# Kernel optimization log

Hardware: AMD Instinct MI355X
Metric: run time of the kernel (lower is better)

The kernel has to match this reference:

```python
import jax, jax.numpy as jnp
import numpy as np

N_NODES = 100000
N_EDGES = 3200000
F_IN = 128
F_OUT = 16


def setup_inputs() -> dict:
    key = jax.random.key(0)
    k1, k2, k3, k4, k5 = jax.random.split(key, 5)
    x = jax.random.normal(k1, (N_NODES, F_IN), dtype=jnp.float32)
    edge_index = jax.random.randint(k2, (2, N_EDGES), 0, N_NODES, dtype=jnp.int64)
    edge_weights = jax.random.uniform(k3, (N_EDGES,), dtype=jnp.float32)
    W = jax.random.normal(k4, (F_IN, F_OUT), dtype=jnp.float32) / np.sqrt(F_IN)
    b = jax.random.normal(k5, (F_OUT,), dtype=jnp.float32)
    return {"x": x, "edge_index": edge_index, "edge_weights": edge_weights, "W": W, "b": b}


def reference(x, edge_index, edge_weights, W, b):
    # GCNConv: out = D^{-1/2} (A + I) D^{-1/2} X W + b  (weighted edges, self-loops)
    n = x.shape[0]
    row = edge_index[0]  # source nodes
    col = edge_index[1]  # target nodes (aggregation destination)
    # add self-loops with weight 1.0 (GCNConv default)
    loop = jnp.arange(n, dtype=row.dtype)
    row_f = jnp.concatenate([row, loop])
    col_f = jnp.concatenate([col, loop])
    ew = jnp.concatenate([edge_weights, jnp.ones((n,), dtype=edge_weights.dtype)])
    # symmetric normalization: deg over destination, norm = d^{-1/2}[row] * w * d^{-1/2}[col]
    deg = jax.ops.segment_sum(ew, col_f, num_segments=n)
    dinv = jnp.where(deg > 0, jax.lax.rsqrt(deg), 0.0)
    norm = dinv[row_f] * ew * dinv[col_f]  # [E+N]
    h = x @ W  # [N, F_OUT] dense projection before propagation
    msgs = h[row_f] * norm[:, None]  # gather + scale, [E+N, F_OUT]
    out = jax.ops.segment_sum(msgs, col_f, num_segments=n)  # scatter-add
    return out + b
```

## Files before the change

### kernel.cpp

```cpp
#include <hip/hip_runtime.h>

#define N_NODES 100000
#define N_EDGES 3200000
#define F_IN 128
#define F_OUT 16

#define NSEG 512
#define EPS (N_EDGES / NSEG)
#define EPT 13
#define NBUCK 512
#define NPB 196
#define CAPR 7424
#define RPT 29
#define GEMM32 ((N_NODES + 31) / 32)
#define PULL_BLOCKS 2048

#define OFF_CUR   0x000000u
#define OFF_NPTR  0x010000u
#define OFF_NCNT  0x080000u
#define OFF_DINV  0x0F0000u
#define OFF_HH    0x160000u
#define OFF_GG    0x780000u
#define OFF_CSR   0xB00000u
#define WS_NEEDED ((size_t)0x1000000 + (size_t)N_EDGES * 8)

__device__ __forceinline__ unsigned short f2bf(float f) {
    unsigned u = __float_as_uint(f);
    unsigned r = (u + 0x7FFFu + ((u >> 16) & 1u)) >> 16;
    return (unsigned short)r;
}
__device__ __forceinline__ float bf2f(unsigned short v) {
    return __uint_as_float((unsigned)v << 16);
}


__global__ void __launch_bounds__(512) k_binA(const int* __restrict__ row,
                                              const int* __restrict__ col,
                                              const float* __restrict__ ew,
                                              int* __restrict__ cursor,
                                              int2* __restrict__ csr,
                                              const float* __restrict__ x,
                                              const float* __restrict__ W,
                                              float* __restrict__ h) {
    __shared__ int smem[2048];
    int tid = threadIdx.x;
    if (blockIdx.x < NSEG) {
        int* lcnt = smem;
        int* gofs = smem + 512;
        int e0 = blockIdx.x * EPS;
        lcnt[tid] = 0;
        __syncthreads();

        int2 rec[EPT];
        int meta[EPT];
#pragma unroll
        for (int k = 0; k < EPT; ++k) {
            int i = k * 512 + tid;
            if (k < EPT - 1 || i < EPS) {
                int e = e0 + i;
                int r = row[e];
                int c = col[e];
                float w = ew[e];
                int bk = c / NPB;
                int pos = atomicAdd(&lcnt[bk], 1);
                rec[k] = make_int2((r << 8) | (c - bk * NPB), __float_as_int(w));
                meta[k] = (bk << 16) | pos;
            }
        }
        __syncthreads();

        int v = lcnt[tid];
        gofs[tid] = tid * CAPR + atomicAdd(&cursor[tid], v);
        __syncthreads();

#pragma unroll
        for (int k = 0; k < EPT; ++k) {
            int i = k * 512 + tid;
            if (k < EPT - 1 || i < EPS) {
                int m = meta[k];
                csr[gofs[m >> 16] + (m & 0xFFFF)] = rec[k];
            }
        }
    } else {
        float* Ws = (float*)smem;
        for (int i = tid; i < F_IN * F_OUT; i += 512) Ws[i] = W[i];
        __syncthreads();
        int n = (blockIdx.x - NSEG) * 32 + (tid >> 4);
        int j = tid & 15;
        if (n >= N_NODES) return;
        const float4* xr = (const float4*)(x + (size_t)n * F_IN);
        float acc = 0.0f;
#pragma unroll
        for (int k4 = 0; k4 < F_IN / 4; ++k4) {
            float4 xv = xr[k4];
            int k = k4 * 4;
            acc += xv.x * Ws[(k + 0) * F_OUT + j];
            acc += xv.y * Ws[(k + 1) * F_OUT + j];
            acc += xv.z * Ws[(k + 2) * F_OUT + j];
            acc += xv.w * Ws[(k + 3) * F_OUT + j];
        }
        h[(size_t)n * F_OUT + j] = acc;
    }
}

__global__ void __launch_bounds__(256) k_sortB(const int* __restrict__ cursor,
                                               int2* __restrict__ csr,
                                               const float* __restrict__ h,
                                               float* __restrict__ dinv,
                                               unsigned short* __restrict__ gb,
                                               int* __restrict__ nodeptr,
                                               int* __restrict__ ncnt) {
    __shared__ int cnt[256];
    __shared__ int basel[256];
    __shared__ int wtot[4];
    __shared__ float dl[256];
    int tid = threadIdx.x;
    int b = blockIdx.x;
    int c0 = b * NPB;
    int rb = b * CAPR;
    int total = cursor[b];
    if (total > CAPR) total = CAPR;

    cnt[tid] = 0;
    __syncthreads();

    int2 rec[RPT];
    int pos[RPT];
#pragma unroll
    for (int k = 0; k < RPT; ++k) {
        int i = k * 256 + tid;
        if (i < total) {
            rec[k] = csr[rb + i];
            pos[k] = atomicAdd(&cnt[rec[k].x & 255], 1);
        }
    }
    __syncthreads();

    int v = cnt[tid];
    int inc = v;
#pragma unroll
    for (int off = 1; off < 64; off <<= 1) {
        int t = __shfl_up(inc, off);
        if ((tid & 63) >= off) inc += t;
    }
    if ((tid & 63) == 63) wtot[tid >> 6] = inc;
    __syncthreads();
    int woff = 0;
#pragma unroll
    for (int k = 0; k < 4; ++k)
        if (k < (tid >> 6)) woff += wtot[k];
    int excl = woff + inc - v;
    int n = c0 + tid;
    if (tid < NPB && n < N_NODES) {
        nodeptr[n] = rb + excl;
        ncnt[n] = v;
    }
    basel[tid] = excl;
    __syncthreads();

#pragma unroll
    for (int k = 0; k < RPT; ++k) {
        int i = k * 256 + tid;
        if (i < total) {
            int cl = rec[k].x & 255;
            csr[rb + basel[cl] + pos[k]] = make_int2(rec[k].x >> 8, rec[k].y);
        }
    }
    __syncthreads();

    float d = 0.0f;
    if (tid < NPB && n < N_NODES) {
        float s0 = 1.0f, s1 = 0.0f, s2 = 0.0f, s3 = 0.0f;
        const int2* run = csr + rb + excl;
        int k = 0;
        for (; k + 4 <= v; k += 4) {
            s0 += __int_as_float(run[k + 0].y);
            s1 += __int_as_float(run[k + 1].y);
            s2 += __int_as_float(run[k + 2].y);
            s3 += __int_as_float(run[k + 3].y);
        }
        for (; k < v; ++k) s0 += __int_as_float(run[k].y);
        float s = (s0 + s1) + (s2 + s3);
        d = rsqrtf(s);
        dinv[n] = d;
    }
    dl[tid] = d;
    __syncthreads();
    for (int i = tid; i < NPB * F_OUT; i += 256) {
        int idx = c0 * F_OUT + i;
        if (idx < N_NODES * F_OUT) gb[idx] = f2bf(dl[i >> 4] * h[idx]);
    }
}

__global__ void __launch_bounds__(256) k_pull5(const int* __restrict__ nodeptr,
                                               const int* __restrict__ ncnt,
                                               const int2* __restrict__ csr,
                                               const unsigned short* __restrict__ gb,
                                               const float* __restrict__ dinv,
                                               const float* __restrict__ bias,
                                               float* __restrict__ out) {
    int wid = threadIdx.x >> 6;
    int lane = threadIdx.x & 63;
    int half = lane >> 5;
    int l32 = lane & 31;
    int l4 = lane & 15;
    int fr = ((l4 & 1) << 3) | ((l4 & 2) << 1) | ((l4 & 4) >> 1) | ((l4 & 8) >> 3);
    float bj = bias[fr];
    const int NPAIR = (N_NODES + 1) / 2;
    for (int q = blockIdx.x * 4 + wid; q < NPAIR; q += PULL_BLOCKS * 4) {
        int n = q * 2 + half;
        bool valid = (n < N_NODES);
        int p0 = valid ? nodeptr[n] : 0;
        int c = valid ? ncnt[n] : 0;
        float acc[16];
#pragma unroll
        for (int k = 0; k < 16; ++k) acc[k] = 0.0f;
        int2 rec = (l32 < c) ? csr[p0 + l32] : make_int2(0, 0);
        for (int base = 0; base < c; base += 32) {
            int2 cur = rec;
            int ni = base + 32 + l32;
            rec = (ni < c) ? csr[p0 + ni] : make_int2(0, 0);
            float w = __int_as_float(cur.y);
            const uint4* gr = (const uint4*)(gb + ((size_t)cur.x << 4));
            uint4 qa = gr[0];
            uint4 qb = gr[1];
            acc[0]  += w * __uint_as_float(qa.x << 16);
            acc[1]  += w * __uint_as_float(qa.x & 0xFFFF0000u);
            acc[2]  += w * __uint_as_float(qa.y << 16);
            acc[3]  += w * __uint_as_float(qa.y & 0xFFFF0000u);
            acc[4]  += w * __uint_as_float(qa.z << 16);
            acc[5]  += w * __uint_as_float(qa.z & 0xFFFF0000u);
            acc[6]  += w * __uint_as_float(qa.w << 16);
            acc[7]  += w * __uint_as_float(qa.w & 0xFFFF0000u);
            acc[8]  += w * __uint_as_float(qb.x << 16);
            acc[9]  += w * __uint_as_float(qb.x & 0xFFFF0000u);
            acc[10] += w * __uint_as_float(qb.y << 16);
            acc[11] += w * __uint_as_float(qb.y & 0xFFFF0000u);
            acc[12] += w * __uint_as_float(qb.z << 16);
            acc[13] += w * __uint_as_float(qb.z & 0xFFFF0000u);
            acc[14] += w * __uint_as_float(qb.w << 16);
            acc[15] += w * __uint_as_float(qb.w & 0xFFFF0000u);
        }
        bool b1 = (lane & 1) != 0;
#pragma unroll
        for (int k = 0; k < 8; ++k) {
            float keep = b1 ? acc[k + 8] : acc[k];
            float send = b1 ? acc[k] : acc[k + 8];
            acc[k] = keep + __shfl_xor(send, 1);
        }
        bool b2 = (lane & 2) != 0;
#pragma unroll
        for (int k = 0; k < 4; ++k) {
            float keep = b2 ? acc[k + 4] : acc[k];
            float send = b2 ? acc[k] : acc[k + 4];
            acc[k] = keep + __shfl_xor(send, 2);
        }
        bool b4 = (lane & 4) != 0;
#pragma unroll
        for (int k = 0; k < 2; ++k) {
            float keep = b4 ? acc[k + 2] : acc[k];
            float send = b4 ? acc[k] : acc[k + 2];
            acc[k] = keep + __shfl_xor(send, 4);
        }
        bool b8 = (lane & 8) != 0;
        {
            float keep = b8 ? acc[1] : acc[0];
            float send = b8 ? acc[0] : acc[1];
            acc[0] = keep + __shfl_xor(send, 8);
        }
        acc[0] += __shfl_xor(acc[0], 16);
        if (l32 < 16 && valid) {
            float d = dinv[n];
            float gs = bf2f(gb[(size_t)n * F_OUT + fr]);
            out[(size_t)n * F_OUT + fr] = bj + d * (gs + acc[0]);
        }
    }
}


#define EDGE_BLOCKS_FB ((N_EDGES + 255) / 256)
#define GEMM_BLOCKS_FB ((N_NODES + 15) / 16)
__global__ void k_init_fb(float* __restrict__ deg) {
    int i = blockIdx.x * blockDim.x + threadIdx.x;
    if (i < N_NODES) deg[i] = 1.0f;
}
__global__ void k_fused_fb(const int* __restrict__ col, const float* __restrict__ ew,
                           float* __restrict__ deg, const float* __restrict__ x,
                           const float* __restrict__ W, float* __restrict__ h) {
    int b3 = blockIdx.x / 3;
    int r3 = blockIdx.x % 3;
    if (r3 < 2) {
        int e = (b3 * 2 + r3) * 256 + threadIdx.x;
        if (e < N_EDGES) atomicAdd(&deg[col[e]], ew[e]);
    } else {
        __shared__ float Ws[F_IN * F_OUT];
        int tid = threadIdx.x;
        for (int i = tid; i < F_IN * F_OUT; i += 256) Ws[i] = W[i];
        __syncthreads();
        int n = b3 * 16 + (tid >> 4);
        int j = tid & 15;
        if (n >= N_NODES) return;
        const float4* xr = (const float4*)(x + (size_t)n * F_IN);
        float acc = 0.0f;
#pragma unroll
        for (int k4 = 0; k4 < F_IN / 4; ++k4) {
            float4 xv = xr[k4];
            int k = k4 * 4;
            acc += xv.x * Ws[(k + 0) * F_OUT + j];
            acc += xv.y * Ws[(k + 1) * F_OUT + j];
            acc += xv.z * Ws[(k + 2) * F_OUT + j];
            acc += xv.w * Ws[(k + 3) * F_OUT + j];
        }
        h[(size_t)n * F_OUT + j] = acc;
    }
}
__global__ void k_final_fb(float* __restrict__ deg, const float* __restrict__ h,
                           const float* __restrict__ b, float* __restrict__ g,
                           float* __restrict__ out) {
    int i = blockIdx.x * blockDim.x + threadIdx.x;
    int n = i >> 4;
    int j = i & 15;
    if (n >= N_NODES) return;
    float d = rsqrtf(deg[n]);
    if (j == 0) deg[n] = d;
    float gg = d * h[i];
    g[i] = gg;
    out[i] = b[j] + d * gg;
}
__global__ void k_scatter_fb(const int* __restrict__ row, const int* __restrict__ col,
                             const float* __restrict__ ew, const float* __restrict__ dinv,
                             const float* __restrict__ g, float* __restrict__ out) {
    long long tid = (long long)blockIdx.x * blockDim.x + threadIdx.x;
    int e = (int)(tid >> 4);
    int j = (int)(tid & 15);
    if (e >= N_EDGES) return;
    int c = col[e];
    float norm = ew[e] * dinv[c];
    atomicAdd(&out[(size_t)c * F_OUT + j], g[(size_t)row[e] * F_OUT + j] * norm);
}

extern "C" void kernel_launch(void* const* d_in, const int* in_sizes, int n_in,
                              void* d_out, int out_size, void* d_ws, size_t ws_size,
                              hipStream_t stream) {
    const float* x  = (const float*)d_in[0];
    const int*   ei = (const int*)d_in[1];
    const float* ew = (const float*)d_in[2];
    const float* W  = (const float*)d_in[3];
    const float* b  = (const float*)d_in[4];
    float* out = (float*)d_out;

    const int* row = ei;
    const int* col = ei + N_EDGES;

    char* ws = (char*)d_ws;
    dim3 blk(256);

    if (ws_size >= WS_NEEDED) {
        int*   cur  = (int*)(ws + OFF_CUR);
        int*   nptr = (int*)(ws + OFF_NPTR);
        int*   ncnt = (int*)(ws + OFF_NCNT);
        float* dinv = (float*)(ws + OFF_DINV);
        float* h    = (float*)(ws + OFF_HH);
        unsigned short* gb = (unsigned short*)(ws + OFF_GG);
        int2*  csr  = (int2*)(ws + OFF_CSR);

        hipMemsetAsync(cur, 0, NBUCK * sizeof(int), stream);
        k_binA<<<NSEG + GEMM32, 512, 0, stream>>>(row, col, ew, cur, csr, x, W, h);
        k_sortB<<<NBUCK, blk, 0, stream>>>(cur, csr, h, dinv, gb, nptr, ncnt);
        k_pull5<<<PULL_BLOCKS, blk, 0, stream>>>(nptr, ncnt, csr, gb, dinv, b, out);
    } else {
        float* deg = (float*)ws;
        float* h   = (float*)(ws + (1u << 20));
        float* g   = (float*)(ws + (8u << 20));
        k_init_fb<<<(N_NODES + 255) / 256, blk, 0, stream>>>(deg);
        k_fused_fb<<<EDGE_BLOCKS_FB + GEMM_BLOCKS_FB, blk, 0, stream>>>(col, ew, deg, x, W, h);
        k_final_fb<<<(N_NODES * F_OUT + 255) / 256, blk, 0, stream>>>(deg, h, b, g, out);
        long long total = (long long)N_EDGES * F_OUT;
        k_scatter_fb<<<(unsigned)((total + 255) / 256), blk, 0, stream>>>(row, col, ew, deg, g, out);
    }
}
```

Baseline: 224.4 us.

## Fuse bin, sort, and pull stages into one cooperative kernel with grid syncs

Replaces the memset plus three kernel launches with a single cooperative kernel of 512 blocks of 512 threads. It zeroes the cursors, bins edges, computes the projection, sorts each bucket and builds the degree normalisation, then runs the pull aggregation, with grid-wide syncs between stages. The goal is to remove launch gaps and the memset. In exchange the whole job runs on only 512 blocks, giving less parallelism than the original 2048-block pull and separate GEMM blocks, and it adds grid-sync overhead. The old launch path is kept as a fallback if the cooperative launch fails.

```diff
diff --git a/kernel.cpp b/kernel.cpp
--- a/kernel.cpp
+++ b/kernel.cpp
@@ -1,4 +1,7 @@
 #include <hip/hip_runtime.h>
+#include <hip/hip_cooperative_groups.h>
+
+namespace cg = cooperative_groups;
 
 #define N_NODES 100000
 #define N_EDGES 3200000
@@ -11,9 +14,11 @@
 #define NBUCK 512
 #define NPB 196
 #define CAPR 7424
-#define RPT 29
+#define RPT 15
+#define RPT3 29
 #define GEMM32 ((N_NODES + 31) / 32)
 #define PULL_BLOCKS 2048
+#define NPAIR ((N_NODES + 1) / 2)
 
 #define OFF_CUR   0x000000u
 #define OFF_NPTR  0x010000u
@@ -31,6 +36,262 @@
 }
 __device__ __forceinline__ float bf2f(unsigned short v) {
     return __uint_as_float((unsigned)v << 16);
+}
+
+
+__global__ void __launch_bounds__(512, 4) k_fused(
+        const int* __restrict__ row, const int* __restrict__ col,
+        const float* __restrict__ ew, int* __restrict__ cursor,
+        int2* __restrict__ csr, const float* __restrict__ x,
+        const float* __restrict__ W, float* __restrict__ h,
+        float* __restrict__ dinv, unsigned short* __restrict__ gb,
+        int* __restrict__ nodeptr, int* __restrict__ ncnt,
+        const float* __restrict__ bias, float* __restrict__ out) {
+    __shared__ int smem[2048];
+    __shared__ int cnt[256];
+    __shared__ int basel[256];
+    __shared__ int wtot4[4];
+    __shared__ float dl[256];
+    cg::grid_group grid = cg::this_grid();
+    int tid = threadIdx.x;
+    int b = blockIdx.x;
+
+    if (tid == 0) atomicExch(&cursor[b], 0);
+    grid.sync();
+    __threadfence();
+
+    {
+        int* lcnt = smem;
+        int* gofs = smem + 512;
+        int e0 = b * EPS;
+        lcnt[tid] = 0;
+        __syncthreads();
+
+        int2 rec[EPT];
+        int meta[EPT];
+#pragma unroll
+        for (int k = 0; k < EPT; ++k) {
+            int i = k * 512 + tid;
+            if (k < EPT - 1 || i < EPS) {
+                int e = e0 + i;
+                int r = row[e];
+                int c = col[e];
+                float w = ew[e];
+                int bk = c / NPB;
+                int pos = atomicAdd(&lcnt[bk], 1);
+                rec[k] = make_int2((r << 8) | (c - bk * NPB), __float_as_int(w));
+                meta[k] = (bk << 16) | pos;
+            }
+        }
+        __syncthreads();
+
+        int v = lcnt[tid];
+        gofs[tid] = tid * CAPR + atomicAdd(&cursor[tid], v);
+        __syncthreads();
+
+#pragma unroll
+        for (int k = 0; k < EPT; ++k) {
+            int i = k * 512 + tid;
+            if (k < EPT - 1 || i < EPS) {
+                int m = meta[k];
+                csr[gofs[m >> 16] + (m & 0xFFFF)] = rec[k];
+            }
+        }
+        __syncthreads();
+    }
+
+    {
+        float* Ws = (float*)smem;
+        for (int i = tid; i < F_IN * F_OUT; i += 512) Ws[i] = W[i];
+        __syncthreads();
+        int j = tid & 15;
+        int nl = tid >> 4;
+        for (int g = b; g < GEMM32; g += NSEG) {
+            int n = g * 32 + nl;
+            if (n < N_NODES) {
+                const float4* xr = (const float4*)(x + (size_t)n * F_IN);
+                float acc = 0.0f;
+#pragma unroll
+                for (int k4 = 0; k4 < F_IN / 4; ++k4) {
+                    float4 xv = xr[k4];
+                    int k = k4 * 4;
+                    acc += xv.x * Ws[(k + 0) * F_OUT + j];
+                    acc += xv.y * Ws[(k + 1) * F_OUT + j];
+                    acc += xv.z * Ws[(k + 2) * F_OUT + j];
+                    acc += xv.w * Ws[(k + 3) * F_OUT + j];
+                }
+                h[(size_t)n * F_OUT + j] = acc;
+            }
+        }
+    }
+
+    __threadfence();
+    grid.sync();
+    __threadfence();
+
+    {
+        int c0 = b * NPB;
+        int rb = b * CAPR;
+        int total = cursor[b];
+        if (total > CAPR) total = CAPR;
+
+        if (tid < 256) cnt[tid] = 0;
+        __syncthreads();
+
+        int2 rec[RPT];
+        int pos[RPT];
+#pragma unroll
+        for (int k = 0; k < RPT; ++k) {
+            int i = k * 512 + tid;
+            if (i < total) {
+                rec[k] = csr[rb + i];
+                pos[k] = atomicAdd(&cnt[rec[k].x & 255], 1);
+            }
+        }
+        __syncthreads();
+
+        int v = 0, inc = 0;
+        if (tid < 256) {
+            v = cnt[tid];
+            inc = v;
+#pragma unroll
+            for (int off = 1; off < 64; off <<= 1) {
+                int t = __shfl_up(inc, off);
+                if ((tid & 63) >= off) inc += t;
+            }
+            if ((tid & 63) == 63) wtot4[tid >> 6] = inc;
+        }
+        __syncthreads();
+        int excl = 0;
+        if (tid < 256) {
+            int woff = 0;
+#pragma unroll
+            for (int k = 0; k < 4; ++k)
+                if (k < (tid >> 6)) woff += wtot4[k];
+            excl = woff + inc - v;
+            int n = c0 + tid;
+            if (tid < NPB && n < N_NODES) {
+                nodeptr[n] = rb + excl;
+                ncnt[n] = v;
+            }
+            basel[tid] = excl;
+        }
+        __syncthreads();
+
+#pragma unroll
+        for (int k = 0; k < RPT; ++k) {
+            int i = k * 512 + tid;
+            if (i < total) {
+                int cl = rec[k].x & 255;
+                csr[rb + basel[cl] + pos[k]] = make_int2(rec[k].x >> 8, rec[k].y);
+            }
+        }
+        __syncthreads();
+
+        float d = 0.0f;
+        if (tid < NPB && (c0 + tid) < N_NODES) {
+            float s0 = 1.0f, s1 = 0.0f, s2 = 0.0f, s3 = 0.0f;
+            const int2* run = csr + rb + excl;
+            int k = 0;
+            for (; k + 4 <= v; k += 4) {
+                s0 += __int_as_float(run[k + 0].y);
+                s1 += __int_as_float(run[k + 1].y);
+                s2 += __int_as_float(run[k + 2].y);
+                s3 += __int_as_float(run[k + 3].y);
+            }
+            for (; k < v; ++k) s0 += __int_as_float(run[k].y);
+            d = rsqrtf((s0 + s1) + (s2 + s3));
+            dinv[c0 + tid] = d;
+        }
+        if (tid < 256) dl[tid] = d;
+        __syncthreads();
+        for (int i = tid; i < NPB * F_OUT; i += 512) {
+            int idx = c0 * F_OUT + i;
+            if (idx < N_NODES * F_OUT) gb[idx] = f2bf(dl[i >> 4] * h[idx]);
+        }
+    }
+
+    __threadfence();
+    grid.sync();
+    __threadfence();
+
+    {
+        int gw = b * 8 + (tid >> 6);
+        int lane = tid & 63;
+        int half = lane >> 5;
+        int l32 = lane & 31;
+        int l4 = lane & 15;
+        int fr = ((l4 & 1) << 3) | ((l4 & 2) << 1) | ((l4 & 4) >> 1) | ((l4 & 8) >> 3);
+        float bj = bias[fr];
+        for (int q = gw; q < NPAIR; q += NSEG * 8) {
+            int n = q * 2 + half;
+            bool valid = (n < N_NODES);
+            int p0 = valid ? nodeptr[n] : 0;
+            int c = valid ? ncnt[n] : 0;
+            float acc[16];
+#pragma unroll
+            for (int k = 0; k < 16; ++k) acc[k] = 0.0f;
+            int2 rec = (l32 < c) ? csr[p0 + l32] : make_int2(0, 0);
+            for (int base = 0; base < c; base += 32) {
+                int2 cur = rec;
+                int ni = base + 32 + l32;
+                rec = (ni < c) ? csr[p0 + ni] : make_int2(0, 0);
+                float w = __int_as_float(cur.y);
+                const uint4* gr = (const uint4*)(gb + ((size_t)cur.x << 4));
+                uint4 qa = gr[0];
+                uint4 qb = gr[1];
+                acc[0]  += w * __uint_as_float(qa.x << 16);
+                acc[1]  += w * __uint_as_float(qa.x & 0xFFFF0000u);
+                acc[2]  += w * __uint_as_float(qa.y << 16);
+                acc[3]  += w * __uint_as_float(qa.y & 0xFFFF0000u);
+                acc[4]  += w * __uint_as_float(qa.z << 16);
+                acc[5]  += w * __uint_as_float(qa.z & 0xFFFF0000u);
+                acc[6]  += w * __uint_as_float(qa.w << 16);
+                acc[7]  += w * __uint_as_float(qa.w & 0xFFFF0000u);
+                acc[8]  += w * __uint_as_float(qb.x << 16);
+                acc[9]  += w * __uint_as_float(qb.x & 0xFFFF0000u);
+                acc[10] += w * __uint_as_float(qb.y << 16);
+                acc[11] += w * __uint_as_float(qb.y & 0xFFFF0000u);
+                acc[12] += w * __uint_as_float(qb.z << 16);
+                acc[13] += w * __uint_as_float(qb.z & 0xFFFF0000u);
+                acc[14] += w * __uint_as_float(qb.w << 16);
+                acc[15] += w * __uint_as_float(qb.w & 0xFFFF0000u);
+            }
+            bool b1 = (lane & 1) != 0;
+#pragma unroll
+            for (int k = 0; k < 8; ++k) {
+                float keep = b1 ? acc[k + 8] : acc[k];
+                float send = b1 ? acc[k] : acc[k + 8];
+                acc[k] = keep + __shfl_xor(send, 1);
+            }
+            bool b2 = (lane & 2) != 0;
+#pragma unroll
+            for (int k = 0; k < 4; ++k) {
+                float keep = b2 ? acc[k + 4] : acc[k];
+                float send = b2 ? acc[k] : acc[k + 4];
+                acc[k] = keep + __shfl_xor(send, 2);
+            }
+            bool b4 = (lane & 4) != 0;
+#pragma unroll
+            for (int k = 0; k < 2; ++k) {
+                float keep = b4 ? acc[k + 2] : acc[k];
+                float send = b4 ? acc[k] : acc[k + 2];
+                acc[k] = keep + __shfl_xor(send, 4);
+            }
+            bool b8 = (lane & 8) != 0;
+            {
+                float keep = b8 ? acc[1] : acc[0];
+                float send = b8 ? acc[0] : acc[1];
+                acc[0] = keep + __shfl_xor(send, 8);
+            }
+            acc[0] += __shfl_xor(acc[0], 16);
+            if (l32 < 16 && valid) {
+                float d = dinv[n];
+                float gs = bf2f(gb[(size_t)n * F_OUT + fr]);
+                out[(size_t)n * F_OUT + fr] = bj + d * (gs + acc[0]);
+            }
+        }
+    }
 }
 
 
@@ -50,7 +311,6 @@
         int e0 = blockIdx.x * EPS;
         lcnt[tid] = 0;
         __syncthreads();
-
         int2 rec[EPT];
         int meta[EPT];
 #pragma unroll
@@ -68,11 +328,9 @@
             }
         }
         __syncthreads();
-
         int v = lcnt[tid];
         gofs[tid] = tid * CAPR + atomicAdd(&cursor[tid], v);
         __syncthreads();
-
 #pragma unroll
         for (int k = 0; k < EPT; ++k) {
             int i = k * 512 + tid;
@@ -120,14 +378,12 @@
     int rb = b * CAPR;
     int total = cursor[b];
     if (total > CAPR) total = CAPR;
-
     cnt[tid] = 0;
     __syncthreads();
-
-    int2 rec[RPT];
-    int pos[RPT];
-#pragma unroll
-    for (int k = 0; k < RPT; ++k) {
+    int2 rec[RPT3];
+    int pos[RPT3];
+#pragma unroll
+    for (int k = 0; k < RPT3; ++k) {
         int i = k * 256 + tid;
         if (i < total) {
             rec[k] = csr[rb + i];
@@ -135,7 +391,6 @@
         }
     }
     __syncthreads();
-
     int v = cnt[tid];
     int inc = v;
 #pragma unroll
@@ -157,9 +412,8 @@
     }
     basel[tid] = excl;
     __syncthreads();
-
-#pragma unroll
-    for (int k = 0; k < RPT; ++k) {
+#pragma unroll
+    for (int k = 0; k < RPT3; ++k) {
         int i = k * 256 + tid;
         if (i < total) {
             int cl = rec[k].x & 255;
@@ -167,7 +421,6 @@
         }
     }
     __syncthreads();
-
     float d = 0.0f;
     if (tid < NPB && n < N_NODES) {
         float s0 = 1.0f, s1 = 0.0f, s2 = 0.0f, s3 = 0.0f;
@@ -180,8 +433,7 @@
             s3 += __int_as_float(run[k + 3].y);
         }
         for (; k < v; ++k) s0 += __int_as_float(run[k].y);
-        float s = (s0 + s1) + (s2 + s3);
-        d = rsqrtf(s);
+        d = rsqrtf((s0 + s1) + (s2 + s3));
         dinv[n] = d;
     }
     dl[tid] = d;
@@ -206,7 +458,6 @@
     int l4 = lane & 15;
     int fr = ((l4 & 1) << 3) | ((l4 & 2) << 1) | ((l4 & 4) >> 1) | ((l4 & 8) >> 3);
     float bj = bias[fr];
-    const int NPAIR = (N_NODES + 1) / 2;
     for (int q = blockIdx.x * 4 + wid; q < NPAIR; q += PULL_BLOCKS * 4) {
         int n = q * 2 + half;
         bool valid = (n < N_NODES);
@@ -364,10 +615,19 @@
         unsigned short* gb = (unsigned short*)(ws + OFF_GG);
         int2*  csr  = (int2*)(ws + OFF_CSR);
 
-        hipMemsetAsync(cur, 0, NBUCK * sizeof(int), stream);
-        k_binA<<<NSEG + GEMM32, 512, 0, stream>>>(row, col, ew, cur, csr, x, W, h);
-        k_sortB<<<NBUCK, blk, 0, stream>>>(cur, csr, h, dinv, gb, nptr, ncnt);
-        k_pull5<<<PULL_BLOCKS, blk, 0, stream>>>(nptr, ncnt, csr, gb, dinv, b, out);
+        void* args[] = {(void*)&row, (void*)&col, (void*)&ew, (void*)&cur,
+                        (void*)&csr, (void*)&x, (void*)&W, (void*)&h,
+                        (void*)&dinv, (void*)&gb, (void*)&nptr, (void*)&ncnt,
+                        (void*)&b, (void*)&out};
+        hipError_t e = hipLaunchCooperativeKernel((const void*)k_fused,
+                                                  dim3(NSEG), dim3(512),
+                                                  args, 0, stream);
+        if (e != hipSuccess) {
+            hipMemsetAsync(cur, 0, NBUCK * sizeof(int), stream);
+            k_binA<<<NSEG + GEMM32, 512, 0, stream>>>(row, col, ew, cur, csr, x, W, h);
+            k_sortB<<<NBUCK, blk, 0, stream>>>(cur, csr, h, dinv, gb, nptr, ncnt);
+            k_pull5<<<PULL_BLOCKS, blk, 0, stream>>>(nptr, ncnt, csr, gb, dinv, b, out);
+        }
     } else {
         float* deg = (float*)ws;
         float* h   = (float*)(ws + (1u << 20));
```

Measured after the change: 783.9 us. 249% more time.
